# Kernel optimization log

Measured on AMD Instinct MI355X. Metric: run time of the kernel, lower is better.

The kernel has to match this reference:

```python
import jax, jax.numpy as jnp
import numpy as np

B, T, C, H = 4, 2048, 1024, 16
D = C // H  # head dim 64


def setup_inputs() -> dict:
    key = jax.random.key(0)
    ks = jax.random.split(key, 5)
    s = 1.0 / np.sqrt(C)
    return {
        "x": jax.random.normal(ks[0], (B, T, C), jnp.float32),
        "Wq": jax.random.normal(ks[1], (C, C), jnp.float32) * s,
        "bq": jnp.zeros((C,), jnp.float32),
        "Wk": jax.random.normal(ks[2], (C, C), jnp.float32) * s,
        "bk": jnp.zeros((C,), jnp.float32),
        "Wv": jax.random.normal(ks[3], (C, C), jnp.float32) * s,
        "bv": jnp.zeros((C,), jnp.float32),
        "Wp": jax.random.normal(ks[4], (C, C), jnp.float32) * s,
        "bp": jnp.zeros((C,), jnp.float32),
    }


def reference(x, Wq, bq, Wk, bk, Wv, bv, Wp, bp):
    # project and split heads: [B,T,C] -> [B,H,T,D]
    def heads(w, b):
        return (x @ w.T + b).reshape(B, T, H, D).transpose(0, 2, 1, 3)

    q = heads(Wq, bq)
    k = heads(Wk, bk)
    v = heads(Wv, bv)

    att = jnp.einsum("bhqd,bhkd->bhqk", q, k) * (1.0 / np.sqrt(D))
    causal = jnp.tril(jnp.ones((T, T), bool))  # [T,T]
    att = jnp.where(causal[None, None], att, -jnp.inf)
    att = jax.nn.softmax(att, axis=-1)
    # dropout prob is 0.0 -> identity
    y = jnp.einsum("bhqk,bhkd->bhqd", att, v)
    y = y.transpose(0, 2, 1, 3).reshape(B, T, C)
    return y @ Wp.T + bp
```

## Files before the change

kernel.cpp:

```cpp
#include <hip/hip_runtime.h>
#include <hip/hip_bf16.h>

#define BB 4
#define TT 2048
#define CC 1024
#define HH 16
#define DD 64
#define PSTR 80

typedef unsigned short u16;
typedef __attribute__((ext_vector_type(8))) short bf16x8;
typedef __attribute__((ext_vector_type(4))) float f32x4;

__device__ __forceinline__ float bf2f(u16 v) {
    union { unsigned u; float f; } c; c.u = ((unsigned)v) << 16; return c.f;
}
__device__ __forceinline__ u16 f2bf(float f) {
    union { float f; unsigned u; } c; c.f = f;
    unsigned u = c.u + 0x7fffu + ((c.u >> 16) & 1u);
    return (u16)(u >> 16);
}
__device__ __forceinline__ float fast_exp2(float x) {
    float r;
    asm volatile("v_exp_f32 %0, %1\n\ts_nop 1" : "=v"(r) : "v"(x));
    return r;
}
__device__ __forceinline__ unsigned pack_bf16(unsigned b0, unsigned b1) {
    unsigned d;
    asm("v_perm_b32 %0, %1, %2, %3" : "=v"(d) : "v"(b1), "v"(b0), "v"(0x07060302u));
    return d;
}
__device__ __forceinline__ uint2 pack4(float v0, float v1, float v2, float v3) {
    uint2 pk;
    pk.x = pack_bf16(__float_as_uint(v0) + 0x8000u, __float_as_uint(v1) + 0x8000u);
    pk.y = pack_bf16(__float_as_uint(v2) + 0x8000u, __float_as_uint(v3) + 0x8000u);
    return pk;
}
__device__ __forceinline__ void gload16(const u16* g, u16* l) {
    __builtin_amdgcn_global_load_lds(
        (const __attribute__((address_space(1))) void*)g,
        (__attribute__((address_space(3))) void*)l, 16, 0, 0);
}

__global__ void detect_dtype(const u16* __restrict__ x, int* __restrict__ flag) {
    __shared__ int cnt;
    if (threadIdx.x == 0) cnt = 0;
    __syncthreads();
    int local = 0;
    for (int i = 0; i < 16; i++) {
        u16 h = x[(threadIdx.x * 16 + i) * 2];
        int e = (h >> 7) & 0xFF;
        if (e >= 118 && e <= 132) local++;
    }
    atomicAdd(&cnt, local);
    __syncthreads();
    if (threadIdx.x == 0) *flag = (cnt >= 2048) ? 1 : 0;
}

struct CastArgs {
    const void* src[9];
    u16* dst[9];
    int blk_start[10];
    int n[9];
};
__global__ __launch_bounds__(256) void cast_all(CastArgs a, const int* __restrict__ flag) {
    int b = blockIdx.x;
    int s = 0;
    while (s < 8 && b >= a.blk_start[s + 1]) s++;
    int i0 = (b - a.blk_start[s]) * 2048 + threadIdx.x * 8;
    if (i0 + 8 > a.n[s]) return;
    if (*flag) {
        *(uint4*)&a.dst[s][i0] = *(const uint4*)&((const u16*)a.src[s])[i0];
    } else {
        const float* sp = (const float*)a.src[s];
        u16 tmp[8];
#pragma unroll
        for (int j = 0; j < 8; j++) tmp[j] = f2bf(sp[i0 + j]);
        *(uint4*)&a.dst[s][i0] = *(uint4*)tmp;
    }
}

__device__ __forceinline__ void gemm_core(
    const u16* __restrict__ X, const u16* __restrict__ W,
    u16* Als, u16* Bls, f32x4 (&acc)[4][4],
    int m0, int n0, int wave, int lane, int quad, int l16, int wm, int wn)
{
    int srow[4], sch[4];
#pragma unroll
    for (int c = 0; c < 4; c++) {
        srow[c] = wave * 32 + c * 8 + (lane >> 3);
        sch[c]  = (lane & 7) ^ (srow[c] & 7);
    }

    for (int k0 = 0; k0 < CC; k0 += 64) {
        __syncthreads();
#pragma unroll
        for (int c = 0; c < 4; c++) {
            gload16(&X[(size_t)(m0 + srow[c]) * CC + k0 + sch[c] * 8],
                    &Als[wave * 2048 + c * 512]);
            gload16(&W[(size_t)(n0 + srow[c]) * CC + k0 + sch[c] * 8],
                    &Bls[wave * 2048 + c * 512]);
        }
        __syncthreads();

#pragma unroll
        for (int kk = 0; kk < 2; kk++) {
            const int sw = ((kk * 4 + quad) ^ (l16 & 7)) * 8;
            bf16x8 a[4], b[4];
#pragma unroll
            for (int i = 0; i < 4; i++)
                a[i] = *(const bf16x8*)&Als[(wm + i * 16 + l16) * 64 + sw];
#pragma unroll
            for (int j = 0; j < 4; j++)
                b[j] = *(const bf16x8*)&Bls[(wn + j * 16 + l16) * 64 + sw];
#pragma unroll
            for (int i = 0; i < 4; i++)
#pragma unroll
                for (int j = 0; j < 4; j++)
                    acc[i][j] = __builtin_amdgcn_mfma_f32_16x16x32_bf16(
                        b[j], a[i], acc[i][j], 0, 0, 0);
        }
    }
}

__global__ __launch_bounds__(256) void gemm_qkv(
    const u16* __restrict__ X,
    const u16* __restrict__ Wq, const u16* __restrict__ Wk, const u16* __restrict__ Wv,
    const u16* __restrict__ bq, const u16* __restrict__ bk, const u16* __restrict__ bv,
    u16* __restrict__ Q, u16* __restrict__ K, u16* __restrict__ VT)
{
    __shared__ __align__(16) u16 Als[128 * 64];
    __shared__ __align__(16) u16 Bls[128 * 64];

    const int tid  = threadIdx.x;
    const int wave = tid >> 6;
    const int lane = tid & 63;
    const int quad = lane >> 4;
    const int l16  = lane & 15;
    const int m0   = blockIdx.x * 128;
    const int n0   = blockIdx.y * 128;
    const int z    = blockIdx.z;
    const int wm   = (wave >> 1) * 64;
    const int wn   = (wave & 1) * 64;

    const u16* W    = (z == 0) ? Wq : (z == 1) ? Wk : Wv;
    const u16* bias = (z == 0) ? bq : (z == 1) ? bk : bv;

    f32x4 acc[4][4];
#pragma unroll
    for (int i = 0; i < 4; i++)
#pragma unroll
        for (int j = 0; j < 4; j++) acc[i][j] = (f32x4)0.0f;

    gemm_core(X, W, Als, Bls, acc, m0, n0, wave, lane, quad, l16, wm, wn);

    const float scale = (z == 0) ? 0.18033688f : 1.0f;
    u16* outp = (z == 0) ? Q : (z == 1) ? K : VT;

#pragma unroll
    for (int j = 0; j < 4; j++) {
        const int n_base = n0 + wn + j * 16 + quad * 4;
        union { uint2 u; u16 us[4]; } braw;
        braw.u = *(const uint2*)&bias[n_base];
        float bvv[4];
#pragma unroll
        for (int r = 0; r < 4; r++) bvv[r] = bf2f(braw.us[r]);
        const int hh = n_base >> 6, d0 = n_base & 63;
#pragma unroll
        for (int i = 0; i < 4; i++) {
            const int m = m0 + wm + i * 16 + l16;
            const int bb = m >> 11, t = m & (TT - 1);
            float v0 = (acc[i][j][0] + bvv[0]) * scale;
            float v1 = (acc[i][j][1] + bvv[1]) * scale;
            float v2 = (acc[i][j][2] + bvv[2]) * scale;
            float v3 = (acc[i][j][3] + bvv[3]) * scale;
            if (z < 2) {
                *(uint2*)&outp[((size_t)(bb * HH + hh) * TT + t) * DD + d0] =
                    pack4(v0, v1, v2, v3);
            } else {
                const size_t base = (size_t)(bb * HH + hh) * DD * TT + t;
                outp[base + (size_t)(d0 + 0) * TT] = f2bf(v0);
                outp[base + (size_t)(d0 + 1) * TT] = f2bf(v1);
                outp[base + (size_t)(d0 + 2) * TT] = f2bf(v2);
                outp[base + (size_t)(d0 + 3) * TT] = f2bf(v3);
            }
        }
    }
}

__global__ __launch_bounds__(256) void gemm_proj(
    const u16* __restrict__ X, const u16* __restrict__ W,
    const u16* __restrict__ bias, void* __restrict__ out,
    const int* __restrict__ flag)
{
    __shared__ __align__(16) u16 Als[128 * 64];
    __shared__ __align__(16) u16 Bls[128 * 64];

    const int tid  = threadIdx.x;
    const int wave = tid >> 6;
    const int lane = tid & 63;
    const int quad = lane >> 4;
    const int l16  = lane & 15;
    const int m0   = blockIdx.x * 128;
    const int n0   = blockIdx.y * 128;
    const int wm   = (wave >> 1) * 64;
    const int wn   = (wave & 1) * 64;
    const int isbf = *flag;

    f32x4 acc[4][4];
#pragma unroll
    for (int i = 0; i < 4; i++)
#pragma unroll
        for (int j = 0; j < 4; j++) acc[i][j] = (f32x4)0.0f;

    gemm_core(X, W, Als, Bls, acc, m0, n0, wave, lane, quad, l16, wm, wn);

#pragma unroll
    for (int j = 0; j < 4; j++) {
        const int n_base = n0 + wn + j * 16 + quad * 4;
        union { uint2 u; u16 us[4]; } braw;
        braw.u = *(const uint2*)&bias[n_base];
        float bvv[4];
#pragma unroll
        for (int r = 0; r < 4; r++) bvv[r] = bf2f(braw.us[r]);
#pragma unroll
        for (int i = 0; i < 4; i++) {
            const int m = m0 + wm + i * 16 + l16;
            float v0 = acc[i][j][0] + bvv[0];
            float v1 = acc[i][j][1] + bvv[1];
            float v2 = acc[i][j][2] + bvv[2];
            float v3 = acc[i][j][3] + bvv[3];
            if (isbf) {
                *(uint2*)&((u16*)out)[(size_t)m * CC + n_base] = pack4(v0, v1, v2, v3);
            } else {
                float4 f; f.x = v0; f.y = v1; f.z = v2; f.w = v3;
                *(float4*)&((float*)out)[(size_t)m * CC + n_base] = f;
            }
        }
    }
}

__global__ __launch_bounds__(256) void attn_kernel(
    const u16* __restrict__ Qg, const u16* __restrict__ Kg,
    const u16* __restrict__ VTg, u16* __restrict__ Yg)
{
    __shared__ __align__(16) u16 Qs[128 * 64];
    __shared__ __align__(16) u16 Ks[64 * 64];
    __shared__ __align__(16) u16 VTs[64 * 64];
    __shared__ __align__(16) u16 Ps[128 * PSTR];
    __shared__ float ls[128];

    const int tid  = threadIdx.x;
    const int wave = tid >> 6;
    const int lane = tid & 63;
    const int quad = lane >> 4;
    const int l16  = lane & 15;
    const int bh    = blockIdx.x;
    const int qtile = (TT / 128 - 1) - blockIdx.y;
    const int h = bh & (HH - 1);
    const int b = bh >> 4;
    const int q0 = qtile * 128;

    const int sch = (lane & 7) ^ (lane >> 3);

    const u16* kp[2];
    const u16* vp[2];
#pragma unroll
    for (int c = 0; c < 2; c++) {
        const int srow = wave * 16 + c * 8 + (lane >> 3);
        kp[c] = Kg + (size_t)bh * TT * DD + (size_t)srow * DD + sch * 8;
        vp[c] = VTg + (size_t)bh * DD * TT + (size_t)srow * TT + sch * 8;
    }

#pragma unroll
    for (int c = 0; c < 4; c++) {
        const int srow = wave * 32 + c * 8 + (lane >> 3);
        gload16(&Qg[((size_t)bh * TT + q0 + srow) * DD + sch * 8],
                &Qs[wave * 2048 + c * 512]);
    }
    __syncthreads();
    bf16x8 qf[2][2];
#pragma unroll
    for (int g = 0; g < 2; g++)
#pragma unroll
        for (int ks = 0; ks < 2; ks++)
            qf[g][ks] = *(const bf16x8*)&Qs[(wave * 32 + g * 16 + l16) * 64 +
                                            ((ks * 4 + quad) ^ (l16 & 7)) * 8];

    f32x4 o_acc[2][4];
#pragma unroll
    for (int g = 0; g < 2; g++)
#pragma unroll
        for (int jt = 0; jt < 4; jt++) o_acc[g][jt] = (f32x4)0.0f;
    float lsum[2] = {0.0f, 0.0f};

    const int ntiles = 2 * qtile;

    for (int kv = 0; kv < ntiles + 2; kv++) {
        const bool masked = (kv >= ntiles);
        __syncthreads();
#pragma unroll
        for (int c = 0; c < 2; c++) {
            gload16(kp[c], &Ks[wave * 1024 + c * 512]);
            gload16(vp[c], &VTs[wave * 1024 + c * 512]);
            kp[c] += 64 * DD;
            vp[c] += 64;
        }
        __syncthreads();

        f32x4 st[2][4];
#pragma unroll
        for (int g = 0; g < 2; g++)
#pragma unroll
            for (int j = 0; j < 4; j++) st[g][j] = (f32x4)0.0f;
#pragma unroll
        for (int ks = 0; ks < 2; ks++) {
            const int rsw = ((ks * 4 + quad) ^ (l16 & 7)) * 8;
#pragma unroll
            for (int j = 0; j < 4; j++) {
                bf16x8 kf = *(const bf16x8*)&Ks[(j * 16 + l16) * 64 + rsw];
#pragma unroll
                for (int g = 0; g < 2; g++)
                    st[g][j] = __builtin_amdgcn_mfma_f32_16x16x32_bf16(
                        kf, qf[g][ks], st[g][j], 0, 0, 0);
            }
        }

#pragma unroll
        for (int g = 0; g < 2; g++) {
            u16* psrow = &Ps[(wave * 32 + g * 16 + l16) * PSTR];
            const int qrow = q0 + wave * 32 + g * 16 + l16;
            float lp = 0.0f;
#pragma unroll
            for (int j = 0; j < 4; j++) {
                float e0 = fast_exp2(st[g][j][0]);
                float e1 = fast_exp2(st[g][j][1]);
                float e2 = fast_exp2(st[g][j][2]);
                float e3 = fast_exp2(st[g][j][3]);
                if (masked) {
                    const int kc = kv * 64 + j * 16 + quad * 4;
                    if (kc + 0 > qrow) e0 = 0.0f;
                    if (kc + 1 > qrow) e1 = 0.0f;
                    if (kc + 2 > qrow) e2 = 0.0f;
                    if (kc + 3 > qrow) e3 = 0.0f;
                }
                lp += (e0 + e1) + (e2 + e3);
                uint2 pk;
                pk.x = pack_bf16(__float_as_uint(e0) + 0x8000u,
                                 __float_as_uint(e1) + 0x8000u);
                pk.y = pack_bf16(__float_as_uint(e2) + 0x8000u,
                                 __float_as_uint(e3) + 0x8000u);
                *(uint2*)&psrow[j * 16 + quad * 4] = pk;
            }
            lsum[g] += lp;
        }

#pragma unroll
        for (int g = 0; g < 2; g++) {
#pragma unroll
            for (int ks = 0; ks < 2; ks++) {
                bf16x8 pf = *(const bf16x8*)&Ps[(wave * 32 + g * 16 + l16) * PSTR +
                                                ks * 32 + quad * 8];
                const int rsw = ((ks * 4 + quad) ^ (l16 & 7)) * 8;
#pragma unroll
                for (int jt = 0; jt < 4; jt++) {
                    bf16x8 vf = *(const bf16x8*)&VTs[(jt * 16 + l16) * 64 + rsw];
                    o_acc[g][jt] = __builtin_amdgcn_mfma_f32_16x16x32_bf16(
                        pf, vf, o_acc[g][jt], 0, 0, 0);
                }
            }
        }
    }

#pragma unroll
    for (int g = 0; g < 2; g++) {
        lsum[g] += __shfl_xor(lsum[g], 16, 64);
        lsum[g] += __shfl_xor(lsum[g], 32, 64);
        ls[wave * 32 + g * 16 + l16] = lsum[g];
    }

#pragma unroll
    for (int g = 0; g < 2; g++) {
        float linv[4];
#pragma unroll
        for (int r = 0; r < 4; r++)
            linv[r] = 1.0f / fmaxf(ls[wave * 32 + g * 16 + quad * 4 + r], 1e-20f);
#pragma unroll
        for (int jt = 0; jt < 4; jt++) {
#pragma unroll
            for (int r = 0; r < 4; r++) {
                const int t = q0 + wave * 32 + g * 16 + quad * 4 + r;
                const int c = h * DD + jt * 16 + l16;
                Yg[((size_t)b * TT + t) * CC + c] = f2bf(o_acc[g][jt][r] * linv[r]);
            }
        }
    }
}

extern "C" void kernel_launch(void* const* d_in, const int* in_sizes, int n_in,
                              void* d_out, int out_size, void* d_ws, size_t ws_size,
                              hipStream_t stream) {
    u16* w = (u16*)d_ws;
    int* flag = (int*)d_ws;
    size_t off = 128;
    const size_t NX = (size_t)BB * TT * CC;
    const size_t NW = (size_t)CC * CC;
    const size_t NB = CC;
    const size_t per = (size_t)BB * HH * TT * DD;

    u16* xb  = w + off; off += NX;
    u16* Wqb = w + off; off += NW;
    u16* Wkb = w + off; off += NW;
    u16* Wvb = w + off; off += NW;
    u16* Wpb = w + off; off += NW;
    u16* bqb = w + off; off += NB;
    u16* bkb = w + off; off += NB;
    u16* bvb = w + off; off += NB;
    u16* bpb = w + off; off += NB;
    u16* Q   = w + off; off += per;
    u16* K   = w + off; off += per;
    u16* VT  = w + off; off += per;
    u16* Y   = w + off; off += per;

    detect_dtype<<<1, 256, 0, stream>>>((const u16*)d_in[0], flag);

    CastArgs ca;
    const int srcmap[9] = {0, 1, 3, 5, 7, 2, 4, 6, 8};
    u16* dsts[9] = {xb, Wqb, Wkb, Wvb, Wpb, bqb, bkb, bvb, bpb};
    int ns[9] = {(int)NX, (int)NW, (int)NW, (int)NW, (int)NW,
                 (int)NB, (int)NB, (int)NB, (int)NB};
    int acc_blk = 0;
    for (int i = 0; i < 9; i++) {
        ca.src[i] = d_in[srcmap[i]];
        ca.dst[i] = dsts[i];
        ca.n[i]   = ns[i];
        ca.blk_start[i] = acc_blk;
        acc_blk += (ns[i] + 2047) / 2048;
    }
    ca.blk_start[9] = acc_blk;
    cast_all<<<acc_blk, 256, 0, stream>>>(ca, flag);

    gemm_qkv<<<dim3(64, 8, 3), 256, 0, stream>>>(xb, Wqb, Wkb, Wvb,
                                                 bqb, bkb, bvb, Q, K, VT);
    attn_kernel<<<dim3(BB * HH, TT / 128), 256, 0, stream>>>(Q, K, VT, Y);
    gemm_proj<<<dim3(64, 8), 256, 0, stream>>>(Y, Wpb, bpb, d_out, flag);
}
```

Before: 261.6 us.

## Use 32x32 MFMA in GEMMs, fold dtype detection into kernels, trim attention LDS

The GEMM core moves from 16x16x32 to 32x32x16 bf16 MFMA tiles, with new epilogue indexing for the 32x32 accumulator layout. The separate dtype-detection launch is dropped; each cast and projection block now probes the input itself with a ballot. The attention kernel loads Q fragments straight from global memory instead of staging them in LDS, hoists V fragment loads out of the row-group loop, shrinks the P stride and adds occupancy hints to the launch bounds. This removes one launch and some LDS traffic, at the cost of every block repeating the detection probe and possible LDS bank conflicts from the new stride.

Measured after the change: 253.6 us. 1.03x faster.

```diff
diff --git a/kernel.cpp b/kernel.cpp
--- a/kernel.cpp
+++ b/kernel.cpp
@@ -6,11 +6,12 @@
 #define CC 1024
 #define HH 16
 #define DD 64
-#define PSTR 80
+#define PSTR 72
 
 typedef unsigned short u16;
 typedef __attribute__((ext_vector_type(8))) short bf16x8;
 typedef __attribute__((ext_vector_type(4))) float f32x4;
+typedef __attribute__((ext_vector_type(16))) float f32x16;
 
 __device__ __forceinline__ float bf2f(u16 v) {
     union { unsigned u; float f; } c; c.u = ((unsigned)v) << 16; return c.f;
@@ -42,19 +43,14 @@
         (__attribute__((address_space(3))) void*)l, 16, 0, 0);
 }
 
-__global__ void detect_dtype(const u16* __restrict__ x, int* __restrict__ flag) {
-    __shared__ int cnt;
-    if (threadIdx.x == 0) cnt = 0;
+__device__ __forceinline__ int detect_bf16(const u16* __restrict__ xprobe, int* sh) {
+    const int t = threadIdx.x;
+    u16 hh = xprobe[2 * t];
+    int e = (hh >> 7) & 0xFF;
+    unsigned long long m = __ballot(e >= 118 && e <= 132);
+    if ((t & 63) == 0) sh[t >> 6] = __popcll(m);
     __syncthreads();
-    int local = 0;
-    for (int i = 0; i < 16; i++) {
-        u16 h = x[(threadIdx.x * 16 + i) * 2];
-        int e = (h >> 7) & 0xFF;
-        if (e >= 118 && e <= 132) local++;
-    }
-    atomicAdd(&cnt, local);
-    __syncthreads();
-    if (threadIdx.x == 0) *flag = (cnt >= 2048) ? 1 : 0;
+    return (sh[0] + sh[1] + sh[2] + sh[3]) >= 128;
 }
 
 struct CastArgs {
@@ -63,13 +59,15 @@
     int blk_start[10];
     int n[9];
 };
-__global__ __launch_bounds__(256) void cast_all(CastArgs a, const int* __restrict__ flag) {
+__global__ __launch_bounds__(256) void cast_all(CastArgs a, const u16* __restrict__ xprobe) {
+    __shared__ int sh[4];
+    const int isbf = detect_bf16(xprobe, sh);
     int b = blockIdx.x;
     int s = 0;
     while (s < 8 && b >= a.blk_start[s + 1]) s++;
     int i0 = (b - a.blk_start[s]) * 2048 + threadIdx.x * 8;
     if (i0 + 8 > a.n[s]) return;
-    if (*flag) {
+    if (isbf) {
         *(uint4*)&a.dst[s][i0] = *(const uint4*)&((const u16*)a.src[s])[i0];
     } else {
         const float* sp = (const float*)a.src[s];
@@ -82,9 +80,11 @@
 
 __device__ __forceinline__ void gemm_core(
     const u16* __restrict__ X, const u16* __restrict__ W,
-    u16* Als, u16* Bls, f32x4 (&acc)[4][4],
-    int m0, int n0, int wave, int lane, int quad, int l16, int wm, int wn)
+    u16* Als, u16* Bls, f32x16 (&acc)[2][2],
+    int m0, int n0, int wave, int lane, int wm, int wn)
 {
+    const int l32 = lane & 31;
+    const int hv  = lane >> 5;
     int srow[4], sch[4];
 #pragma unroll
     for (int c = 0; c < 4; c++) {
@@ -104,26 +104,26 @@
         __syncthreads();
 
 #pragma unroll
-        for (int kk = 0; kk < 2; kk++) {
-            const int sw = ((kk * 4 + quad) ^ (l16 & 7)) * 8;
-            bf16x8 a[4], b[4];
-#pragma unroll
-            for (int i = 0; i < 4; i++)
-                a[i] = *(const bf16x8*)&Als[(wm + i * 16 + l16) * 64 + sw];
-#pragma unroll
-            for (int j = 0; j < 4; j++)
-                b[j] = *(const bf16x8*)&Bls[(wn + j * 16 + l16) * 64 + sw];
-#pragma unroll
-            for (int i = 0; i < 4; i++)
-#pragma unroll
-                for (int j = 0; j < 4; j++)
-                    acc[i][j] = __builtin_amdgcn_mfma_f32_16x16x32_bf16(
+        for (int ks = 0; ks < 4; ks++) {
+            const int sw = ((ks * 2 + hv) ^ (l32 & 7)) * 8;
+            bf16x8 a[2], b[2];
+#pragma unroll
+            for (int i = 0; i < 2; i++)
+                a[i] = *(const bf16x8*)&Als[(wm + i * 32 + l32) * 64 + sw];
+#pragma unroll
+            for (int j = 0; j < 2; j++)
+                b[j] = *(const bf16x8*)&Bls[(wn + j * 32 + l32) * 64 + sw];
+#pragma unroll
+            for (int i = 0; i < 2; i++)
+#pragma unroll
+                for (int j = 0; j < 2; j++)
+                    acc[i][j] = __builtin_amdgcn_mfma_f32_32x32x16_bf16(
                         b[j], a[i], acc[i][j], 0, 0, 0);
         }
     }
 }
 
-__global__ __launch_bounds__(256) void gemm_qkv(
+__global__ __launch_bounds__(256, 4) void gemm_qkv(
     const u16* __restrict__ X,
     const u16* __restrict__ Wq, const u16* __restrict__ Wk, const u16* __restrict__ Wv,
     const u16* __restrict__ bq, const u16* __restrict__ bk, const u16* __restrict__ bv,
@@ -135,8 +135,8 @@
     const int tid  = threadIdx.x;
     const int wave = tid >> 6;
     const int lane = tid & 63;
-    const int quad = lane >> 4;
-    const int l16  = lane & 15;
+    const int l32  = lane & 31;
+    const int hv   = lane >> 5;
     const int m0   = blockIdx.x * 128;
     const int n0   = blockIdx.y * 128;
     const int z    = blockIdx.z;
@@ -146,105 +146,106 @@
     const u16* W    = (z == 0) ? Wq : (z == 1) ? Wk : Wv;
     const u16* bias = (z == 0) ? bq : (z == 1) ? bk : bv;
 
-    f32x4 acc[4][4];
-#pragma unroll
-    for (int i = 0; i < 4; i++)
-#pragma unroll
-        for (int j = 0; j < 4; j++) acc[i][j] = (f32x4)0.0f;
-
-    gemm_core(X, W, Als, Bls, acc, m0, n0, wave, lane, quad, l16, wm, wn);
+    f32x16 acc[2][2];
+#pragma unroll
+    for (int i = 0; i < 2; i++)
+#pragma unroll
+        for (int j = 0; j < 2; j++) acc[i][j] = (f32x16)0.0f;
+
+    gemm_core(X, W, Als, Bls, acc, m0, n0, wave, lane, wm, wn);
 
     const float scale = (z == 0) ? 0.18033688f : 1.0f;
     u16* outp = (z == 0) ? Q : (z == 1) ? K : VT;
 
 #pragma unroll
-    for (int j = 0; j < 4; j++) {
-        const int n_base = n0 + wn + j * 16 + quad * 4;
-        union { uint2 u; u16 us[4]; } braw;
-        braw.u = *(const uint2*)&bias[n_base];
-        float bvv[4];
-#pragma unroll
-        for (int r = 0; r < 4; r++) bvv[r] = bf2f(braw.us[r]);
-        const int hh = n_base >> 6, d0 = n_base & 63;
-#pragma unroll
-        for (int i = 0; i < 4; i++) {
-            const int m = m0 + wm + i * 16 + l16;
-            const int bb = m >> 11, t = m & (TT - 1);
-            float v0 = (acc[i][j][0] + bvv[0]) * scale;
-            float v1 = (acc[i][j][1] + bvv[1]) * scale;
-            float v2 = (acc[i][j][2] + bvv[2]) * scale;
-            float v3 = (acc[i][j][3] + bvv[3]) * scale;
-            if (z < 2) {
-                *(uint2*)&outp[((size_t)(bb * HH + hh) * TT + t) * DD + d0] =
-                    pack4(v0, v1, v2, v3);
-            } else {
-                const size_t base = (size_t)(bb * HH + hh) * DD * TT + t;
-                outp[base + (size_t)(d0 + 0) * TT] = f2bf(v0);
-                outp[base + (size_t)(d0 + 1) * TT] = f2bf(v1);
-                outp[base + (size_t)(d0 + 2) * TT] = f2bf(v2);
-                outp[base + (size_t)(d0 + 3) * TT] = f2bf(v3);
-            }
-        }
-    }
-}
-
-__global__ __launch_bounds__(256) void gemm_proj(
+    for (int j = 0; j < 2; j++) {
+#pragma unroll
+        for (int rq = 0; rq < 4; rq++) {
+            const int n_base = n0 + wn + j * 32 + rq * 8 + hv * 4;
+            union { uint2 u; u16 us[4]; } braw;
+            braw.u = *(const uint2*)&bias[n_base];
+            const int hh = n_base >> 6, d0 = n_base & 63;
+#pragma unroll
+            for (int i = 0; i < 2; i++) {
+                const int m = m0 + wm + i * 32 + l32;
+                const int bb = m >> 11, t = m & (TT - 1);
+                float v0 = (acc[i][j][rq * 4 + 0] + bf2f(braw.us[0])) * scale;
+                float v1 = (acc[i][j][rq * 4 + 1] + bf2f(braw.us[1])) * scale;
+                float v2 = (acc[i][j][rq * 4 + 2] + bf2f(braw.us[2])) * scale;
+                float v3 = (acc[i][j][rq * 4 + 3] + bf2f(braw.us[3])) * scale;
+                if (z < 2) {
+                    *(uint2*)&outp[((size_t)(bb * HH + hh) * TT + t) * DD + d0] =
+                        pack4(v0, v1, v2, v3);
+                } else {
+                    const size_t base = (size_t)(bb * HH + hh) * DD * TT + t;
+                    outp[base + (size_t)(d0 + 0) * TT] = f2bf(v0);
+                    outp[base + (size_t)(d0 + 1) * TT] = f2bf(v1);
+                    outp[base + (size_t)(d0 + 2) * TT] = f2bf(v2);
+                    outp[base + (size_t)(d0 + 3) * TT] = f2bf(v3);
+                }
+            }
+        }
+    }
+}
+
+__global__ __launch_bounds__(256, 4) void gemm_proj(
     const u16* __restrict__ X, const u16* __restrict__ W,
     const u16* __restrict__ bias, void* __restrict__ out,
-    const int* __restrict__ flag)
+    const u16* __restrict__ xprobe)
 {
     __shared__ __align__(16) u16 Als[128 * 64];
     __shared__ __align__(16) u16 Bls[128 * 64];
+    __shared__ int sh[4];
+
+    const int isbf = detect_bf16(xprobe, sh);
 
     const int tid  = threadIdx.x;
     const int wave = tid >> 6;
     const int lane = tid & 63;
-    const int quad = lane >> 4;
-    const int l16  = lane & 15;
+    const int l32  = lane & 31;
+    const int hv   = lane >> 5;
     const int m0   = blockIdx.x * 128;
     const int n0   = blockIdx.y * 128;
     const int wm   = (wave >> 1) * 64;
     const int wn   = (wave & 1) * 64;
-    const int isbf = *flag;
-
-    f32x4 acc[4][4];
-#pragma unroll
-    for (int i = 0; i < 4; i++)
-#pragma unroll
-        for (int j = 0; j < 4; j++) acc[i][j] = (f32x4)0.0f;
-
-    gemm_core(X, W, Als, Bls, acc, m0, n0, wave, lane, quad, l16, wm, wn);
-
-#pragma unroll
-    for (int j = 0; j < 4; j++) {
-        const int n_base = n0 + wn + j * 16 + quad * 4;
-        union { uint2 u; u16 us[4]; } braw;
-        braw.u = *(const uint2*)&bias[n_base];
-        float bvv[4];
-#pragma unroll
-        for (int r = 0; r < 4; r++) bvv[r] = bf2f(braw.us[r]);
-#pragma unroll
-        for (int i = 0; i < 4; i++) {
-            const int m = m0 + wm + i * 16 + l16;
-            float v0 = acc[i][j][0] + bvv[0];
-            float v1 = acc[i][j][1] + bvv[1];
-            float v2 = acc[i][j][2] + bvv[2];
-            float v3 = acc[i][j][3] + bvv[3];
-            if (isbf) {
-                *(uint2*)&((u16*)out)[(size_t)m * CC + n_base] = pack4(v0, v1, v2, v3);
-            } else {
-                float4 f; f.x = v0; f.y = v1; f.z = v2; f.w = v3;
-                *(float4*)&((float*)out)[(size_t)m * CC + n_base] = f;
-            }
-        }
-    }
-}
-
-__global__ __launch_bounds__(256) void attn_kernel(
+
+    f32x16 acc[2][2];
+#pragma unroll
+    for (int i = 0; i < 2; i++)
+#pragma unroll
+        for (int j = 0; j < 2; j++) acc[i][j] = (f32x16)0.0f;
+
+    gemm_core(X, W, Als, Bls, acc, m0, n0, wave, lane, wm, wn);
+
+#pragma unroll
+    for (int j = 0; j < 2; j++) {
+#pragma unroll
+        for (int rq = 0; rq < 4; rq++) {
+            const int n_base = n0 + wn + j * 32 + rq * 8 + hv * 4;
+            union { uint2 u; u16 us[4]; } braw;
+            braw.u = *(const uint2*)&bias[n_base];
+#pragma unroll
+            for (int i = 0; i < 2; i++) {
+                const int m = m0 + wm + i * 32 + l32;
+                float v0 = acc[i][j][rq * 4 + 0] + bf2f(braw.us[0]);
+                float v1 = acc[i][j][rq * 4 + 1] + bf2f(braw.us[1]);
+                float v2 = acc[i][j][rq * 4 + 2] + bf2f(braw.us[2]);
+                float v3 = acc[i][j][rq * 4 + 3] + bf2f(braw.us[3]);
+                if (isbf) {
+                    *(uint2*)&((u16*)out)[(size_t)m * CC + n_base] = pack4(v0, v1, v2, v3);
+                } else {
+                    float4 f; f.x = v0; f.y = v1; f.z = v2; f.w = v3;
+                    *(float4*)&((float*)out)[(size_t)m * CC + n_base] = f;
+                }
+            }
+        }
+    }
+}
+
+__global__ __launch_bounds__(256, 4) void attn_kernel(
     const u16* __restrict__ Qg, const u16* __restrict__ Kg,
     const u16* __restrict__ VTg, u16* __restrict__ Yg)
 {
-    __shared__ __align__(16) u16 Qs[128 * 64];
     __shared__ __align__(16) u16 Ks[64 * 64];
     __shared__ __align__(16) u16 VTs[64 * 64];
     __shared__ __align__(16) u16 Ps[128 * PSTR];
@@ -261,8 +262,15 @@
     const int b = bh >> 4;
     const int q0 = qtile * 128;
 
+    bf16x8 qf[2][2];
+#pragma unroll
+    for (int g = 0; g < 2; g++)
+#pragma unroll
+        for (int ks = 0; ks < 2; ks++)
+            qf[g][ks] = *(const bf16x8*)&Qg[((size_t)bh * TT + q0 + wave * 32 +
+                                             g * 16 + l16) * DD + ks * 32 + quad * 8];
+
     const int sch = (lane & 7) ^ (lane >> 3);
-
     const u16* kp[2];
     const u16* vp[2];
 #pragma unroll
@@ -271,21 +279,6 @@
         kp[c] = Kg + (size_t)bh * TT * DD + (size_t)srow * DD + sch * 8;
         vp[c] = VTg + (size_t)bh * DD * TT + (size_t)srow * TT + sch * 8;
     }
-
-#pragma unroll
-    for (int c = 0; c < 4; c++) {
-        const int srow = wave * 32 + c * 8 + (lane >> 3);
-        gload16(&Qg[((size_t)bh * TT + q0 + srow) * DD + sch * 8],
-                &Qs[wave * 2048 + c * 512]);
-    }
-    __syncthreads();
-    bf16x8 qf[2][2];
-#pragma unroll
-    for (int g = 0; g < 2; g++)
-#pragma unroll
-        for (int ks = 0; ks < 2; ks++)
-            qf[g][ks] = *(const bf16x8*)&Qs[(wave * 32 + g * 16 + l16) * 64 +
-                                            ((ks * 4 + quad) ^ (l16 & 7)) * 8];
 
     f32x4 o_acc[2][4];
 #pragma unroll
@@ -356,18 +349,20 @@
         }
 
 #pragma unroll
-        for (int g = 0; g < 2; g++) {
-#pragma unroll
-            for (int ks = 0; ks < 2; ks++) {
+        for (int ks = 0; ks < 2; ks++) {
+            const int rsw = ((ks * 4 + quad) ^ (l16 & 7)) * 8;
+            bf16x8 vfk[4];
+#pragma unroll
+            for (int jt = 0; jt < 4; jt++)
+                vfk[jt] = *(const bf16x8*)&VTs[(jt * 16 + l16) * 64 + rsw];
+#pragma unroll
+            for (int g = 0; g < 2; g++) {
                 bf16x8 pf = *(const bf16x8*)&Ps[(wave * 32 + g * 16 + l16) * PSTR +
                                                 ks * 32 + quad * 8];
-                const int rsw = ((ks * 4 + quad) ^ (l16 & 7)) * 8;
-#pragma unroll
-                for (int jt = 0; jt < 4; jt++) {
-                    bf16x8 vf = *(const bf16x8*)&VTs[(jt * 16 + l16) * 64 + rsw];
+#pragma unroll
+                for (int jt = 0; jt < 4; jt++)
                     o_acc[g][jt] = __builtin_amdgcn_mfma_f32_16x16x32_bf16(
-                        pf, vf, o_acc[g][jt], 0, 0, 0);
-                }
+                        pf, vfk[jt], o_acc[g][jt], 0, 0, 0);
             }
         }
     }
@@ -401,8 +396,7 @@
                               void* d_out, int out_size, void* d_ws, size_t ws_size,
                               hipStream_t stream) {
     u16* w = (u16*)d_ws;
-    int* flag = (int*)d_ws;
-    size_t off = 128;
+    size_t off = 0;
     const size_t NX = (size_t)BB * TT * CC;
     const size_t NW = (size_t)CC * CC;
     const size_t NB = CC;
@@ -422,8 +416,6 @@
     u16* VT  = w + off; off += per;
     u16* Y   = w + off; off += per;
 
-    detect_dtype<<<1, 256, 0, stream>>>((const u16*)d_in[0], flag);
-
     CastArgs ca;
     const int srcmap[9] = {0, 1, 3, 5, 7, 2, 4, 6, 8};
     u16* dsts[9] = {xb, Wqb, Wkb, Wvb, Wpb, bqb, bkb, bvb, bpb};
@@ -438,10 +430,11 @@
         acc_blk += (ns[i] + 2047) / 2048;
     }
     ca.blk_start[9] = acc_blk;
-    cast_all<<<acc_blk, 256, 0, stream>>>(ca, flag);
+    cast_all<<<acc_blk, 256, 0, stream>>>(ca, (const u16*)d_in[0]);
 
     gemm_qkv<<<dim3(64, 8, 3), 256, 0, stream>>>(xb, Wqb, Wkb, Wvb,
                                                  bqb, bkb, bvb, Q, K, VT);
     attn_kernel<<<dim3(BB * HH, TT / 128), 256, 0, stream>>>(Q, K, VT, Y);
-    gemm_proj<<<dim3(64, 8), 256, 0, stream>>>(Y, Wpb, bpb, d_out, flag);
-}
+    gemm_proj<<<dim3(64, 8), 256, 0, stream>>>(Y, Wpb, bpb, d_out,
+                                               (const u16*)d_in[0]);
+}
```
